# Optimization experiments

Measured on AMD Instinct MI355X. Metric: run time of the kernel, lower is better.

## Reference

```python
import jax, jax.numpy as jnp
import numpy as np

EPS = 1e-12  # matches torch F.normalize default eps

def _l2_normalize(v, axis):
    n = jnp.sqrt(jnp.sum(v * v, axis=axis, keepdims=True))
    return v / jnp.maximum(n, EPS)

def setup_inputs() -> dict:
    key = jax.random.key(0)
    k1, k2, k3 = jax.random.split(key, 3)
    N, C, H, W = 16, 128, 64, 64
    D, K = 512, 64
    x = jax.random.normal(k1, (N, C, H, W), dtype=jnp.float32)
    conv_w = jax.random.normal(k2, (D, C), dtype=jnp.float32) * (1.0 / np.sqrt(C))
    conv_b = jnp.zeros((D,), dtype=jnp.float32)
    centroids = jax.random.uniform(k3, (K, D), dtype=jnp.float32)
    return {"x": x, "conv_w": conv_w, "conv_b": conv_b, "centroids": centroids}

def reference(x, conv_w, conv_b, centroids):
    N, C, H, W = x.shape
    D = conv_w.shape[0]
    # descriptor-wise L2 normalization over channels
    x = _l2_normalize(x, axis=1)
    # 1x1 conv == per-pixel linear projection; flatten spatial -> L = H*W
    f = jnp.einsum('nchw,dc->ndhw', x, conv_w) + conv_b[None, :, None, None]
    f = f.reshape(N, D, H * W)                      # (N, D, L)
    c = _l2_normalize(centroids, axis=1)            # (K, D)
    # soft assignment: dot of normalized centroid with each projected descriptor
    logits = jnp.einsum('kd,ndl->nkl', c, f)        # (N, K, L)
    s = jax.nn.softmax(logits, axis=-1)             # softmax over spatial positions
    # weighted sum of descriptors per cluster (no (N,K,D,L) materialization)
    vlad = jnp.einsum('nkl,ndl->nkd', s, f)         # (N, K, D)
    return vlad
```

## Files before the change

kernel.cpp:

```cpp
#include <hip/hip_runtime.h>

#define NB 16
#define CD 128
#define HW 4096
#define DD 512
#define KC 64

typedef __attribute__((ext_vector_type(8))) short bfrag;
typedef __attribute__((ext_vector_type(4))) float facc;

__device__ __forceinline__ unsigned short f2bf(float f) {
  union { float f; unsigned u; } v; v.f = f;
  unsigned r = v.u + 0x7fffu + ((v.u >> 16) & 1u);
  return (unsigned short)(r >> 16);
}
__device__ __forceinline__ float bf2f(unsigned short h) {
  union { unsigned u; float f; } v; v.u = ((unsigned)h) << 16; return v.f;
}
__device__ __forceinline__ unsigned f2bf2(float lo, float hi) {
  unsigned r;
  asm("v_cvt_pk_bf16_f32 %0, %1, %2" : "=v"(r) : "v"(lo), "v"(hi));
  return r;
}
__device__ __forceinline__ void gll16(const void* g, void* l) {
  __builtin_amdgcn_global_load_lds(
      (__attribute__((address_space(1))) void*)(uintptr_t)g,
      (__attribute__((address_space(3))) void*)(uintptr_t)l, 16, 0, 0);
}
__device__ __forceinline__ int swzr(int r) { return ((r & 7) ^ ((r >> 3) & 7)) << 4; }

__global__ __launch_bounds__(256) void k_prep(const float* __restrict__ conv_w,
                                              const float* __restrict__ conv_b,
                                              const float* __restrict__ centroids,
                                              unsigned short* __restrict__ Wsw,
                                              unsigned short* __restrict__ Mg,
                                              float* __restrict__ bk) {
  int b = blockIdx.x, t = threadIdx.x;
  if (b < KC) {
    __shared__ float red[4];
    __shared__ float sinv;
    __shared__ float mred[256];
    const float* row = centroids + (size_t)b * DD;
    float v0 = row[t], v1 = row[t + 256];
    float ss = v0 * v0 + v1 * v1;
    #pragma unroll
    for (int off = 32; off; off >>= 1) ss += __shfl_xor(ss, off);
    if ((t & 63) == 0) red[t >> 6] = ss;
    __syncthreads();
    if (t == 0) sinv = 1.0f / fmaxf(sqrtf(red[0] + red[1] + red[2] + red[3]), 1e-12f);
    __syncthreads();
    float inv = sinv;
    int dd = t >> 7, c = t & 127;
    float macc = 0.f;
    #pragma unroll 8
    for (int d0 = 0; d0 < DD; d0 += 2) {
      float cn = row[d0 + dd];
      macc += cn * conv_w[(size_t)(d0 + dd) * CD + c];
    }
    mred[t] = macc;
    float bp = v0 * conv_b[t] + v1 * conv_b[t + 256];
    #pragma unroll
    for (int off = 32; off; off >>= 1) bp += __shfl_xor(bp, off);
    if ((t & 63) == 0) red[t >> 6] = bp;
    __syncthreads();
    if (t < 128) Mg[(size_t)b * CD + t] = f2bf((mred[t] + mred[t + 128]) * inv);
    if (t == 0) bk[b] = (red[0] + red[1] + red[2] + red[3]) * inv;
  } else {
    int i = (b - KC) * 2048 + t * 8;
    const float4* src = (const float4*)(conv_w + i);
    float4 a = src[0], c4 = src[1];
    int d = i >> 7, c0 = i & 127;
    int dch = d >> 6, dl = d & 63;
    uint4 w;
    w.x = f2bf2(a.x, a.y);   w.y = f2bf2(a.z, a.w);
    w.z = f2bf2(c4.x, c4.y); w.w = f2bf2(c4.z, c4.w);
    *(uint4*)((char*)Wsw + dch * 16384 + dl * 256 + ((c0 * 2) ^ swzr(dl))) = w;
  }
}

__global__ __launch_bounds__(512, 2) void k_xproj(const float* __restrict__ x,
                                                  const unsigned short* __restrict__ Wsw,
                                                  const unsigned short* __restrict__ Mg,
                                                  const float* __restrict__ bk,
                                                  const float* __restrict__ conv_b,
                                                  unsigned short* __restrict__ fT,
                                                  unsigned short* __restrict__ eg,
                                                  float* __restrict__ psums) {
  __shared__ __align__(16) char smem[67072];
  char* Xraw  = smem;
  char* etile = smem;
  char* Ws0   = smem + 32768;
  float* invb = (float*)(smem + 65536);
  float* ps   = (float*)(smem + 66048);
  int n = blockIdx.y, lblk = blockIdx.x, l0 = lblk * 128;
  int t = threadIdx.x, lane = t & 63, wid = t >> 6;

  #pragma unroll
  for (int q = 0; q < 2; q++)
    gll16((const char*)Wsw + (q * 8 + wid) * 1024 + lane * 16, Ws0 + (q * 8 + wid) * 1024);

  #pragma unroll
  for (int j = 0; j < 2; j++) {
    int c0 = ((t >> 4) + 32 * j) * 2;
    const float4* r0p = (const float4*)(x + ((size_t)n * CD + c0) * HW + l0);
    const float4* r1p = (const float4*)(x + ((size_t)n * CD + c0 + 1) * HW + l0);
    #pragma unroll
    for (int jj = 0; jj < 2; jj++) {
      int f4 = (t & 15) + 16 * jj;
      float4 a = r0p[f4], b = r1p[f4];
      int lb = f4 * 4;
      *(unsigned*)(Xraw + (lb + 0) * 256 + ((c0 * 2) ^ swzr(lb + 0))) = f2bf2(a.x, b.x);
      *(unsigned*)(Xraw + (lb + 1) * 256 + ((c0 * 2) ^ swzr(lb + 1))) = f2bf2(a.y, b.y);
      *(unsigned*)(Xraw + (lb + 2) * 256 + ((c0 * 2) ^ swzr(lb + 2))) = f2bf2(a.z, b.z);
      *(unsigned*)(Xraw + (lb + 3) * 256 + ((c0 * 2) ^ swzr(lb + 3))) = f2bf2(a.w, b.w);
    }
  }
  __syncthreads();

  int wd = wid & 1, wl = wid >> 1;
  int ek = wid & 1;
  int r0 = (lane >> 4) << 2, cl = lane & 15;
  int hi8 = (lane >> 4) << 3;

  bfrag ma[4][2];
  #pragma unroll
  for (int kk = 0; kk < 4; kk++)
    #pragma unroll
    for (int m2 = 0; m2 < 2; m2++)
      ma[kk][m2] = *(const bfrag*)(Mg + (size_t)(ek * 32 + m2 * 16 + cl) * CD + kk * 32 + hi8);

  {
    int l = t >> 2;
    float ss = 0.f;
    #pragma unroll
    for (int p = 0; p < 4; p++) {
      int s16 = (t & 3) + 4 * p;
      bfrag v = *(const bfrag*)(Xraw + l * 256 + ((s16 * 16) ^ swzr(l)));
      #pragma unroll
      for (int i = 0; i < 8; i++) { float f = bf2f((unsigned short)v[i]); ss += f * f; }
    }
    ss += __shfl_xor(ss, 1); ss += __shfl_xor(ss, 2);
    if ((t & 3) == 0) invb[l] = 1.0f / fmaxf(sqrtf(ss), 1e-12f);
  }
  __syncthreads();

  bfrag bfh[4][2];
  #pragma unroll
  for (int kk = 0; kk < 4; kk++)
    #pragma unroll
    for (int j = 0; j < 2; j++) {
      int row = wl * 32 + j * 16 + cl;
      int c0e = kk * 32 + hi8;
      bfh[kk][j] = *(const bfrag*)(Xraw + row * 256 + ((c0e * 2) ^ swzr(row)));
    }
  float hinv[2];
  #pragma unroll
  for (int j = 0; j < 2; j++) hinv[j] = invb[wl * 32 + j * 16 + cl];
  __syncthreads();

  facc zero = {0.f, 0.f, 0.f, 0.f};
  facc e_acc[2][2];
  e_acc[0][0] = zero; e_acc[0][1] = zero; e_acc[1][0] = zero; e_acc[1][1] = zero;
  #pragma unroll
  for (int kk = 0; kk < 4; kk++)
    #pragma unroll
    for (int m2 = 0; m2 < 2; m2++)
      #pragma unroll
      for (int j2 = 0; j2 < 2; j2++)
        e_acc[m2][j2] = __builtin_amdgcn_mfma_f32_16x16x32_bf16(ma[kk][m2], bfh[kk][j2], e_acc[m2][j2], 0, 0, 0);

  for (int dch = 0; dch < 8; dch++) {
    const char* Wsb = Ws0 + ((dch & 1) << 14);
    char* fb = smem + ((dch & 1) << 14);
    facc acc[2][2];
    acc[0][0] = zero; acc[0][1] = zero; acc[1][0] = zero; acc[1][1] = zero;
    #pragma unroll
    for (int kk = 0; kk < 4; kk++) {
      int c0e = kk * 32 + hi8;
      bfrag am[2];
      #pragma unroll
      for (int m = 0; m < 2; m++) {
        int d = wd * 32 + m * 16 + cl;
        am[m] = *(const bfrag*)(Wsb + d * 256 + ((c0e * 2) ^ swzr(d)));
      }
      #pragma unroll
      for (int m = 0; m < 2; m++)
        #pragma unroll
        for (int j = 0; j < 2; j++)
          acc[m][j] = __builtin_amdgcn_mfma_f32_16x16x32_bf16(am[m], bfh[kk][j], acc[m][j], 0, 0, 0);
    }
    #pragma unroll
    for (int m = 0; m < 2; m++) {
      int d0 = wd * 32 + m * 16 + r0;
      float4 bq = *(const float4*)(conv_b + dch * 64 + d0);
      #pragma unroll
      for (int j = 0; j < 2; j++) {
        int l = wl * 32 + j * 16 + cl;
        uint2 w;
        w.x = f2bf2(acc[m][j][0] * hinv[j] + bq.x, acc[m][j][1] * hinv[j] + bq.y);
        w.y = f2bf2(acc[m][j][2] * hinv[j] + bq.z, acc[m][j][3] * hinv[j] + bq.w);
        *(uint2*)(fb + l * 128 + ((d0 * 2) ^ swzr(l))) = w;
      }
    }
    if (dch < 7) {
      #pragma unroll
      for (int q = 0; q < 2; q++)
        gll16((const char*)Wsw + (dch + 1) * 16384 + (q * 8 + wid) * 1024 + lane * 16,
              Ws0 + (((dch + 1) & 1) << 14) + (q * 8 + wid) * 1024);
    }
    __builtin_amdgcn_sched_barrier(0);
    if (dch >= 1) {
      const char* fprev = smem + (((dch - 1) & 1) << 14);
      #pragma unroll
      for (int p = 0; p < 2; p++) {
        int ch = p * 512 + t;
        int lr = ch >> 3, c16 = ch & 7;
        bfrag v = *(const bfrag*)(fprev + lr * 128 + ((c16 * 16) ^ swzr(lr)));
        *(bfrag*)(fT + ((size_t)n * HW + l0 + lr) * DD + (dch - 1) * 64 + c16 * 8) = v;
      }
    }
    if (dch == 0) { asm volatile("s_waitcnt vmcnt(0) lgkmcnt(0)" ::: "memory"); }
    else         { asm volatile("s_waitcnt vmcnt(2) lgkmcnt(0)" ::: "memory"); }
    __builtin_amdgcn_s_barrier();
    __builtin_amdgcn_sched_barrier(0);
  }
  {
    const char* fprev = smem + 16384;
    #pragma unroll
    for (int p = 0; p < 2; p++) {
      int ch = p * 512 + t;
      int lr = ch >> 3, c16 = ch & 7;
      bfrag v = *(const bfrag*)(fprev + lr * 128 + ((c16 * 16) ^ swzr(lr)));
      *(bfrag*)(fT + ((size_t)n * HW + l0 + lr) * DD + 7 * 64 + c16 * 8) = v;
    }
  }

  {
    #pragma unroll
    for (int m2 = 0; m2 < 2; m2++) {
      int k20 = ek * 32 + m2 * 16 + r0;
      float4 bkq = *(const float4*)(bk + k20);
      #pragma unroll
      for (int q = 0; q < 4; q++) {
        int k2 = k20 + q;
        float bkv = (q == 0) ? bkq.x : (q == 1) ? bkq.y : (q == 2) ? bkq.z : bkq.w;
        float vsum = 0.f;
        #pragma unroll
        for (int j2 = 0; j2 < 2; j2++) {
          int l2 = wl * 32 + j2 * 16 + cl;
          float ev = __expf(e_acc[m2][j2][q] * hinv[j2] + bkv);
          *(unsigned short*)(etile + (l2 >> 6) * 8192 + k2 * 128 +
                             (((l2 & 63) * 2) ^ swzr(k2))) = f2bf(ev);
          vsum += ev;
        }
        vsum += __shfl_xor(vsum, 1); vsum += __shfl_xor(vsum, 2);
        vsum += __shfl_xor(vsum, 4); vsum += __shfl_xor(vsum, 8);
        if (cl == 0) ps[k2 * 4 + wl] = vsum;
      }
    }
  }
  __syncthreads();
  {
    size_t base = ((size_t)n * 64 + lblk * 2) * 8192;
    #pragma unroll
    for (int p = 0; p < 2; p++) {
      uint4 v = *(const uint4*)(etile + (t + p * 512) * 16);
      *(uint4*)((char*)eg + base + (t + p * 512) * 16) = v;
    }
  }
  if (t < 64) {
    float4 v = ((const float4*)ps)[t];
    psums[((size_t)n * 32 + lblk) * 64 + t] = v.x + v.y + v.z + v.w;
  }
}

__global__ __launch_bounds__(256, 2) void k_vlad(const unsigned short* __restrict__ eg,
                                                 const unsigned short* __restrict__ fT,
                                                 float* __restrict__ part) {
  __shared__ __align__(16) char smem[49152];
  char* As = smem;
  char* Bs = smem + 16384;
  int t = threadIdx.x, lane = t & 63, wid = t >> 6;
  int wr = wid >> 1, wc = wid & 1;
  int lin = blockIdx.x;
  int xcd = lin & 7, jj = lin >> 3;
  int grp = xcd * 16 + (jj >> 2);
  int dt = jj & 3, n = grp >> 3, sk = grp & 7;
  int dbase = dt * 128;
  const unsigned short* fTb = fT + (size_t)n * HW * DD + dbase;
  facc acc[2][4];
  facc zero = {0.f, 0.f, 0.f, 0.f};
  #pragma unroll
  for (int m = 0; m < 2; m++)
    #pragma unroll
    for (int j = 0; j < 4; j++) acc[m][j] = zero;

  bfrag br[8];
  #pragma unroll
  for (int q = 0; q < 8; q++) {
    int ch = q * 256 + t;
    int l = ch >> 4, dc = ch & 15;
    br[q] = *(const bfrag*)(fTb + (size_t)(sk * 512 + l) * DD + dc * 8);
  }

  #pragma unroll
  for (int ks = 0; ks < 4; ks++) {
    int l0 = sk * 512 + ks * 128;
    #pragma unroll
    for (int q = 0; q < 8; q++) {
      int ch = q * 256 + t;
      int l = ch >> 4, dc = ch & 15;
      #pragma unroll
      for (int i = 0; i < 8; i++) {
        int d = dc * 8 + i;
        int swz = (((d & 7) ^ ((d >> 3) & 7)) << 4);
        *(unsigned short*)(Bs + d * 256 + ((l * 2) ^ swz)) = (unsigned short)br[q][i];
      }
    }
    __builtin_amdgcn_sched_barrier(0);
    {
      const char* easrc = (const char*)eg + ((size_t)n * 64 + (l0 >> 6)) * 8192;
      #pragma unroll
      for (int q = 0; q < 4; q++)
        gll16(easrc + (q * 4 + wid) * 1024 + lane * 16, As + (q * 4 + wid) * 1024);
    }
    __builtin_amdgcn_sched_barrier(0);
    if (ks < 3) {
      #pragma unroll
      for (int q = 0; q < 8; q++) {
        int ch = q * 256 + t;
        int l = ch >> 4, dc = ch & 15;
        br[q] = *(const bfrag*)(fTb + (size_t)(l0 + 128 + l) * DD + dc * 8);
      }
      asm volatile("s_waitcnt vmcnt(8) lgkmcnt(0)" ::: "memory");
    } else {
      asm volatile("s_waitcnt vmcnt(0) lgkmcnt(0)" ::: "memory");
    }
    __builtin_amdgcn_s_barrier();
    __builtin_amdgcn_sched_barrier(0);
    #pragma unroll
    for (int kk = 0; kk < 128; kk += 32) {
      int lk = kk + ((lane >> 4) << 3);
      const char* Ai = As + (kk >> 6) * 8192;
      int ll = lk & 63;
      bfrag af[2], bf[4];
      #pragma unroll
      for (int m = 0; m < 2; m++) {
        int krow = wr * 32 + m * 16 + (lane & 15);
        af[m] = *(const bfrag*)(Ai + krow * 128 + ((ll * 2) ^ swzr(krow)));
      }
      #pragma unroll
      for (int j = 0; j < 4; j++) {
        int d = wc * 64 + j * 16 + (lane & 15);
        int swz = (((d & 7) ^ ((d >> 3) & 7)) << 4);
        bf[j] = *(const bfrag*)(Bs + d * 256 + ((lk * 2) ^ swz));
      }
      #pragma unroll
      for (int m = 0; m < 2; m++)
        #pragma unroll
        for (int j = 0; j < 4; j++)
          acc[m][j] = __builtin_amdgcn_mfma_f32_16x16x32_bf16(af[m], bf[j], acc[m][j], 0, 0, 0);
    }
    asm volatile("s_waitcnt lgkmcnt(0)" ::: "memory");
    __builtin_amdgcn_s_barrier();
    __builtin_amdgcn_sched_barrier(0);
  }
  int r0 = (lane >> 4) << 2, cl = lane & 15;
  size_t base = ((size_t)(sk * NB + n)) * (KC * DD);
  #pragma unroll
  for (int m = 0; m < 2; m++) {
    int krow = wr * 32 + m * 16 + r0;
    #pragma unroll
    for (int j = 0; j < 4; j++) {
      int d = dbase + wc * 64 + j * 16 + cl;
      #pragma unroll
      for (int q = 0; q < 4; q++)
        part[base + (size_t)(krow + q) * DD + d] = acc[m][j][q];
    }
  }
}

__global__ __launch_bounds__(256) void k_reduce(const float* __restrict__ part,
                                                const float* __restrict__ psums,
                                                float* __restrict__ out) {
  int b = blockIdx.x, t = threadIdx.x;
  int nk = b >> 1;
  int n = nk >> 6, k = nk & 63;
  __shared__ float rsh;
  if (t < 32) {
    float s = psums[((size_t)n * 32 + t) * 64 + k];
    #pragma unroll
    for (int off = 16; off; off >>= 1) s += __shfl_xor(s, off, 32);
    if (t == 0) rsh = 1.0f / s;
  }
  __syncthreads();
  float rinv = rsh;
  int i = b * 256 + t;
  float s = 0.f;
  #pragma unroll
  for (int skk = 0; skk < 8; skk++) s += part[(size_t)skk * (NB * KC * DD) + i];
  out[i] = s * rinv;
}

extern "C" void kernel_launch(void* const* d_in, const int* in_sizes, int n_in,
                              void* d_out, int out_size, void* d_ws, size_t ws_size,
                              hipStream_t stream) {
  const float* x         = (const float*)d_in[0];
  const float* conv_w    = (const float*)d_in[1];
  const float* conv_b    = (const float*)d_in[2];
  const float* centroids = (const float*)d_in[3];
  float* out = (float*)d_out;
  char* ws = (char*)d_ws;

  unsigned short* Wsw  = (unsigned short*)(ws);
  unsigned short* Mg   = (unsigned short*)(ws + 131072);
  float*          bk   = (float*)(ws + 147456);
  unsigned short* fT   = (unsigned short*)(ws + 148480);
  unsigned short* eg   = (unsigned short*)(ws + 67257344ull);
  float*          psums= (float*)(ws + 75645952ull);
  float*          part = (float*)(ws + 75777024ull);

  k_prep<<<dim3(96), dim3(256), 0, stream>>>(conv_w, conv_b, centroids, Wsw, Mg, bk);

  k_xproj<<<dim3(32, NB), dim3(512), 0, stream>>>(x, Wsw, Mg, bk, conv_b, fT, eg, psums);

  k_vlad<<<dim3(512), dim3(256), 0, stream>>>(eg, fT, part);

  k_reduce<<<dim3(NB * KC * DD / 256), dim3(256), 0, stream>>>(part, psums, out);

  (void)in_sizes; (void)n_in; (void)out_size; (void)ws_size;
}
```

Baseline: 62.36 us.

## Fuse projection, exp-assignment, and VLAD accumulation into one kernel

Merges the projection kernel and the VLAD GEMM kernel so that the projected descriptors and exp-weights stay in shared memory. This removes the round trip of the large bf16 fT tensor and the eg buffer through global memory. Each block now covers 256 spatial positions in four 64-wide sub-tiles and accumulates the partial VLAD in registers. The grid shrinks to 256 blocks with one block per CU, and k_reduce now sums 16 partials instead of 8. In exchange the kernel gives up occupancy, runs more barriers per sub-tile, and loses the overlap of W loads with compute (the W chunks are reloaded for every sub-tile).

```diff
diff --git a/kernel.cpp b/kernel.cpp
--- a/kernel.cpp
+++ b/kernel.cpp
@@ -52,7 +52,7 @@
     float inv = sinv;
     int dd = t >> 7, c = t & 127;
     float macc = 0.f;
-    #pragma unroll 8
+    #pragma unroll 16
     for (int d0 = 0; d0 < DD; d0 += 2) {
       float cn = row[d0 + dd];
       macc += cn * conv_w[(size_t)(d0 + dd) * CD + c];
@@ -78,47 +78,24 @@
   }
 }
 
-__global__ __launch_bounds__(512, 2) void k_xproj(const float* __restrict__ x,
+__global__ __launch_bounds__(512, 1) void k_fused(const float* __restrict__ x,
                                                   const unsigned short* __restrict__ Wsw,
                                                   const unsigned short* __restrict__ Mg,
                                                   const float* __restrict__ bk,
                                                   const float* __restrict__ conv_b,
-                                                  unsigned short* __restrict__ fT,
-                                                  unsigned short* __restrict__ eg,
+                                                  float* __restrict__ part,
                                                   float* __restrict__ psums) {
-  __shared__ __align__(16) char smem[67072];
-  char* Xraw  = smem;
-  char* etile = smem;
-  char* Ws0   = smem + 32768;
-  float* invb = (float*)(smem + 65536);
-  float* ps   = (float*)(smem + 66048);
-  int n = blockIdx.y, lblk = blockIdx.x, l0 = lblk * 128;
+  __shared__ __align__(16) char smem[124160];
+  char* Xsub  = smem;
+  char* ftile = smem + 16384;
+  char* WsB   = smem + 81920;
+  char* etile = smem + 114688;
+  float* invb = (float*)(smem + 122880);
+  float* ps   = (float*)(smem + 123136);
+  int n = blockIdx.y, lblk = blockIdx.x;
   int t = threadIdx.x, lane = t & 63, wid = t >> 6;
-
-  #pragma unroll
-  for (int q = 0; q < 2; q++)
-    gll16((const char*)Wsw + (q * 8 + wid) * 1024 + lane * 16, Ws0 + (q * 8 + wid) * 1024);
-
-  #pragma unroll
-  for (int j = 0; j < 2; j++) {
-    int c0 = ((t >> 4) + 32 * j) * 2;
-    const float4* r0p = (const float4*)(x + ((size_t)n * CD + c0) * HW + l0);
-    const float4* r1p = (const float4*)(x + ((size_t)n * CD + c0 + 1) * HW + l0);
-    #pragma unroll
-    for (int jj = 0; jj < 2; jj++) {
-      int f4 = (t & 15) + 16 * jj;
-      float4 a = r0p[f4], b = r1p[f4];
-      int lb = f4 * 4;
-      *(unsigned*)(Xraw + (lb + 0) * 256 + ((c0 * 2) ^ swzr(lb + 0))) = f2bf2(a.x, b.x);
-      *(unsigned*)(Xraw + (lb + 1) * 256 + ((c0 * 2) ^ swzr(lb + 1))) = f2bf2(a.y, b.y);
-      *(unsigned*)(Xraw + (lb + 2) * 256 + ((c0 * 2) ^ swzr(lb + 2))) = f2bf2(a.z, b.z);
-      *(unsigned*)(Xraw + (lb + 3) * 256 + ((c0 * 2) ^ swzr(lb + 3))) = f2bf2(a.w, b.w);
-    }
-  }
-  __syncthreads();
-
-  int wd = wid & 1, wl = wid >> 1;
-  int ek = wid & 1;
+  int g2 = wid >> 2;
+  int g4 = wid & 3;
   int r0 = (lane >> 4) << 2, cl = lane & 15;
   int hi8 = (lane >> 4) << 3;
 
@@ -127,256 +104,180 @@
   for (int kk = 0; kk < 4; kk++)
     #pragma unroll
     for (int m2 = 0; m2 < 2; m2++)
-      ma[kk][m2] = *(const bfrag*)(Mg + (size_t)(ek * 32 + m2 * 16 + cl) * CD + kk * 32 + hi8);
+      ma[kk][m2] = *(const bfrag*)(Mg + (size_t)(g2 * 32 + m2 * 16 + cl) * CD + kk * 32 + hi8);
+  float4 bkh[2];
+  #pragma unroll
+  for (int m2 = 0; m2 < 2; m2++) bkh[m2] = *(const float4*)(bk + g2 * 32 + m2 * 16 + r0);
+  float bvh[8];
+  #pragma unroll
+  for (int dch = 0; dch < 8; dch++) bvh[dch] = conv_b[dch * 64 + g4 * 16 + cl];
+
+  #pragma unroll
+  for (int q = 0; q < 2; q++)
+    gll16((const char*)Wsw + (q * 8 + wid) * 1024 + lane * 16, WsB + (q * 8 + wid) * 1024);
+
+  facc zero = {0.f, 0.f, 0.f, 0.f};
+  facc acc_v[2][8];
+  #pragma unroll
+  for (int m = 0; m < 2; m++)
+    #pragma unroll
+    for (int j = 0; j < 8; j++) acc_v[m][j] = zero;
+  float rs[2][4] = {{0.f,0.f,0.f,0.f},{0.f,0.f,0.f,0.f}};
+
+  for (int sub = 0; sub < 4; sub++) {
+    int l0 = lblk * 256 + sub * 64;
+    {
+      int c0 = (t >> 3) * 2;
+      const float4* r0p = (const float4*)(x + ((size_t)n * CD + c0) * HW + l0);
+      const float4* r1p = (const float4*)(x + ((size_t)n * CD + c0 + 1) * HW + l0);
+      #pragma unroll
+      for (int jj = 0; jj < 2; jj++) {
+        int f4 = (t & 7) + 8 * jj;
+        float4 a = r0p[f4], b = r1p[f4];
+        int lb = f4 * 4;
+        *(unsigned*)(Xsub + (lb + 0) * 256 + ((c0 * 2) ^ swzr(lb + 0))) = f2bf2(a.x, b.x);
+        *(unsigned*)(Xsub + (lb + 1) * 256 + ((c0 * 2) ^ swzr(lb + 1))) = f2bf2(a.y, b.y);
+        *(unsigned*)(Xsub + (lb + 2) * 256 + ((c0 * 2) ^ swzr(lb + 2))) = f2bf2(a.z, b.z);
+        *(unsigned*)(Xsub + (lb + 3) * 256 + ((c0 * 2) ^ swzr(lb + 3))) = f2bf2(a.w, b.w);
+      }
+    }
+    __syncthreads();
+    {
+      int l = t >> 3;
+      float ss = 0.f;
+      #pragma unroll
+      for (int p = 0; p < 2; p++) {
+        int s16 = (t & 7) + 8 * p;
+        bfrag v = *(const bfrag*)(Xsub + l * 256 + ((s16 * 16) ^ swzr(l)));
+        #pragma unroll
+        for (int i = 0; i < 8; i++) { float f = bf2f((unsigned short)v[i]); ss += f * f; }
+      }
+      ss += __shfl_xor(ss, 1); ss += __shfl_xor(ss, 2); ss += __shfl_xor(ss, 4);
+      if ((t & 7) == 0) invb[l] = 1.0f / fmaxf(sqrtf(ss), 1e-12f);
+    }
+    __syncthreads();
+
+    bfrag bfh[4][2];
+    #pragma unroll
+    for (int kk = 0; kk < 4; kk++)
+      #pragma unroll
+      for (int m = 0; m < 2; m++) {
+        int row = g2 * 32 + m * 16 + cl;
+        bfh[kk][m] = *(const bfrag*)(Xsub + row * 256 + (((kk * 32 + hi8) * 2) ^ swzr(row)));
+      }
+    float hinvq[2][4];
+    #pragma unroll
+    for (int m = 0; m < 2; m++)
+      #pragma unroll
+      for (int q = 0; q < 4; q++) hinvq[m][q] = invb[g2 * 32 + m * 16 + r0 + q];
+    float invl = invb[g4 * 16 + cl];
+
+    facc e_acc[2];
+    e_acc[0] = zero; e_acc[1] = zero;
+    #pragma unroll
+    for (int kk = 0; kk < 4; kk++) {
+      int erow = g4 * 16 + cl;
+      bfrag xe = *(const bfrag*)(Xsub + erow * 256 + (((kk * 32 + hi8) * 2) ^ swzr(erow)));
+      #pragma unroll
+      for (int m2 = 0; m2 < 2; m2++)
+        e_acc[m2] = __builtin_amdgcn_mfma_f32_16x16x32_bf16(ma[kk][m2], xe, e_acc[m2], 0, 0, 0);
+    }
+    #pragma unroll
+    for (int m2 = 0; m2 < 2; m2++) {
+      #pragma unroll
+      for (int q = 0; q < 4; q++) {
+        int k2 = g2 * 32 + m2 * 16 + r0 + q;
+        float bkv = (q == 0) ? bkh[m2].x : (q == 1) ? bkh[m2].y : (q == 2) ? bkh[m2].z : bkh[m2].w;
+        float ev = __expf(e_acc[m2][q] * invl + bkv);
+        int l2 = g4 * 16 + cl;
+        *(unsigned short*)(etile + k2 * 128 + ((l2 * 2) ^ swzr(k2))) = f2bf(ev);
+        rs[m2][q] += ev;
+      }
+    }
+
+    for (int dch = 0; dch < 8; dch++) {
+      {
+        int nxt = (dch + 1) & 7;
+        char* wdst = WsB + (((dch + 1) & 1) << 14);
+        #pragma unroll
+        for (int q = 0; q < 2; q++)
+          gll16((const char*)Wsw + nxt * 16384 + (q * 8 + wid) * 1024 + lane * 16,
+                wdst + (q * 8 + wid) * 1024);
+      }
+      const char* Wsb = WsB + ((dch & 1) << 14);
+      facc fa[2];
+      fa[0] = zero; fa[1] = zero;
+      #pragma unroll
+      for (int kk = 0; kk < 4; kk++) {
+        int drow = g4 * 16 + cl;
+        bfrag wf = *(const bfrag*)(Wsb + drow * 256 + (((kk * 32 + hi8) * 2) ^ swzr(drow)));
+        #pragma unroll
+        for (int m = 0; m < 2; m++)
+          fa[m] = __builtin_amdgcn_mfma_f32_16x16x32_bf16(bfh[kk][m], wf, fa[m], 0, 0, 0);
+      }
+      {
+        int d = dch * 64 + g4 * 16 + cl;
+        float bv = bvh[dch];
+        #pragma unroll
+        for (int m = 0; m < 2; m++) {
+          int lm = g2 * 32 + m * 16 + r0;
+          uint2 w;
+          w.x = f2bf2(fa[m][0] * hinvq[m][0] + bv, fa[m][1] * hinvq[m][1] + bv);
+          w.y = f2bf2(fa[m][2] * hinvq[m][2] + bv, fa[m][3] * hinvq[m][3] + bv);
+          *(uint2*)(ftile + d * 128 + ((lm * 2) ^ swzr(d))) = w;
+        }
+      }
+      __syncthreads();
+    }
+
+    #pragma unroll
+    for (int kk2 = 0; kk2 < 2; kk2++) {
+      int loff = (kk2 * 32 + hi8) * 2;
+      bfrag ae[2];
+      #pragma unroll
+      for (int m = 0; m < 2; m++) {
+        int krow = g2 * 32 + m * 16 + cl;
+        ae[m] = *(const bfrag*)(etile + krow * 128 + (loff ^ swzr(krow)));
+      }
+      #pragma unroll
+      for (int j = 0; j < 8; j++) {
+        int d = g4 * 128 + j * 16 + cl;
+        bfrag bf = *(const bfrag*)(ftile + d * 128 + (loff ^ swzr(d)));
+        #pragma unroll
+        for (int m = 0; m < 2; m++)
+          acc_v[m][j] = __builtin_amdgcn_mfma_f32_16x16x32_bf16(ae[m], bf, acc_v[m][j], 0, 0, 0);
+      }
+    }
+    __syncthreads();
+  }
 
   {
-    int l = t >> 2;
-    float ss = 0.f;
-    #pragma unroll
-    for (int p = 0; p < 4; p++) {
-      int s16 = (t & 3) + 4 * p;
-      bfrag v = *(const bfrag*)(Xraw + l * 256 + ((s16 * 16) ^ swzr(l)));
-      #pragma unroll
-      for (int i = 0; i < 8; i++) { float f = bf2f((unsigned short)v[i]); ss += f * f; }
-    }
-    ss += __shfl_xor(ss, 1); ss += __shfl_xor(ss, 2);
-    if ((t & 3) == 0) invb[l] = 1.0f / fmaxf(sqrtf(ss), 1e-12f);
-  }
+    size_t base = ((size_t)(lblk * NB + n)) * (KC * DD);
+    #pragma unroll
+    for (int m = 0; m < 2; m++) {
+      int krow = g2 * 32 + m * 16 + r0;
+      #pragma unroll
+      for (int j = 0; j < 8; j++) {
+        int d = g4 * 128 + j * 16 + cl;
+        #pragma unroll
+        for (int q = 0; q < 4; q++)
+          part[base + (size_t)(krow + q) * DD + d] = acc_v[m][j][q];
+      }
+    }
+  }
+  #pragma unroll
+  for (int m2 = 0; m2 < 2; m2++)
+    #pragma unroll
+    for (int q = 0; q < 4; q++) {
+      float v = rs[m2][q];
+      v += __shfl_xor(v, 1); v += __shfl_xor(v, 2);
+      v += __shfl_xor(v, 4); v += __shfl_xor(v, 8);
+      if (cl == 0) ps[(g2 * 32 + m2 * 16 + r0 + q) * 4 + g4] = v;
+    }
   __syncthreads();
-
-  bfrag bfh[4][2];
-  #pragma unroll
-  for (int kk = 0; kk < 4; kk++)
-    #pragma unroll
-    for (int j = 0; j < 2; j++) {
-      int row = wl * 32 + j * 16 + cl;
-      int c0e = kk * 32 + hi8;
-      bfh[kk][j] = *(const bfrag*)(Xraw + row * 256 + ((c0e * 2) ^ swzr(row)));
-    }
-  float hinv[2];
-  #pragma unroll
-  for (int j = 0; j < 2; j++) hinv[j] = invb[wl * 32 + j * 16 + cl];
-  __syncthreads();
-
-  facc zero = {0.f, 0.f, 0.f, 0.f};
-  facc e_acc[2][2];
-  e_acc[0][0] = zero; e_acc[0][1] = zero; e_acc[1][0] = zero; e_acc[1][1] = zero;
-  #pragma unroll
-  for (int kk = 0; kk < 4; kk++)
-    #pragma unroll
-    for (int m2 = 0; m2 < 2; m2++)
-      #pragma unroll
-      for (int j2 = 0; j2 < 2; j2++)
-        e_acc[m2][j2] = __builtin_amdgcn_mfma_f32_16x16x32_bf16(ma[kk][m2], bfh[kk][j2], e_acc[m2][j2], 0, 0, 0);
-
-  for (int dch = 0; dch < 8; dch++) {
-    const char* Wsb = Ws0 + ((dch & 1) << 14);
-    char* fb = smem + ((dch & 1) << 14);
-    facc acc[2][2];
-    acc[0][0] = zero; acc[0][1] = zero; acc[1][0] = zero; acc[1][1] = zero;
-    #pragma unroll
-    for (int kk = 0; kk < 4; kk++) {
-      int c0e = kk * 32 + hi8;
-      bfrag am[2];
-      #pragma unroll
-      for (int m = 0; m < 2; m++) {
-        int d = wd * 32 + m * 16 + cl;
-        am[m] = *(const bfrag*)(Wsb + d * 256 + ((c0e * 2) ^ swzr(d)));
-      }
-      #pragma unroll
-      for (int m = 0; m < 2; m++)
-        #pragma unroll
-        for (int j = 0; j < 2; j++)
-          acc[m][j] = __builtin_amdgcn_mfma_f32_16x16x32_bf16(am[m], bfh[kk][j], acc[m][j], 0, 0, 0);
-    }
-    #pragma unroll
-    for (int m = 0; m < 2; m++) {
-      int d0 = wd * 32 + m * 16 + r0;
-      float4 bq = *(const float4*)(conv_b + dch * 64 + d0);
-      #pragma unroll
-      for (int j = 0; j < 2; j++) {
-        int l = wl * 32 + j * 16 + cl;
-        uint2 w;
-        w.x = f2bf2(acc[m][j][0] * hinv[j] + bq.x, acc[m][j][1] * hinv[j] + bq.y);
-        w.y = f2bf2(acc[m][j][2] * hinv[j] + bq.z, acc[m][j][3] * hinv[j] + bq.w);
-        *(uint2*)(fb + l * 128 + ((d0 * 2) ^ swzr(l))) = w;
-      }
-    }
-    if (dch < 7) {
-      #pragma unroll
-      for (int q = 0; q < 2; q++)
-        gll16((const char*)Wsw + (dch + 1) * 16384 + (q * 8 + wid) * 1024 + lane * 16,
-              Ws0 + (((dch + 1) & 1) << 14) + (q * 8 + wid) * 1024);
-    }
-    __builtin_amdgcn_sched_barrier(0);
-    if (dch >= 1) {
-      const char* fprev = smem + (((dch - 1) & 1) << 14);
-      #pragma unroll
-      for (int p = 0; p < 2; p++) {
-        int ch = p * 512 + t;
-        int lr = ch >> 3, c16 = ch & 7;
-        bfrag v = *(const bfrag*)(fprev + lr * 128 + ((c16 * 16) ^ swzr(lr)));
-        *(bfrag*)(fT + ((size_t)n * HW + l0 + lr) * DD + (dch - 1) * 64 + c16 * 8) = v;
-      }
-    }
-    if (dch == 0) { asm volatile("s_waitcnt vmcnt(0) lgkmcnt(0)" ::: "memory"); }
-    else         { asm volatile("s_waitcnt vmcnt(2) lgkmcnt(0)" ::: "memory"); }
-    __builtin_amdgcn_s_barrier();
-    __builtin_amdgcn_sched_barrier(0);
-  }
-  {
-    const char* fprev = smem + 16384;
-    #pragma unroll
-    for (int p = 0; p < 2; p++) {
-      int ch = p * 512 + t;
-      int lr = ch >> 3, c16 = ch & 7;
-      bfrag v = *(const bfrag*)(fprev + lr * 128 + ((c16 * 16) ^ swzr(lr)));
-      *(bfrag*)(fT + ((size_t)n * HW + l0 + lr) * DD + 7 * 64 + c16 * 8) = v;
-    }
-  }
-
-  {
-    #pragma unroll
-    for (int m2 = 0; m2 < 2; m2++) {
-      int k20 = ek * 32 + m2 * 16 + r0;
-      float4 bkq = *(const float4*)(bk + k20);
-      #pragma unroll
-      for (int q = 0; q < 4; q++) {
-        int k2 = k20 + q;
-        float bkv = (q == 0) ? bkq.x : (q == 1) ? bkq.y : (q == 2) ? bkq.z : bkq.w;
-        float vsum = 0.f;
-        #pragma unroll
-        for (int j2 = 0; j2 < 2; j2++) {
-          int l2 = wl * 32 + j2 * 16 + cl;
-          float ev = __expf(e_acc[m2][j2][q] * hinv[j2] + bkv);
-          *(unsigned short*)(etile + (l2 >> 6) * 8192 + k2 * 128 +
-                             (((l2 & 63) * 2) ^ swzr(k2))) = f2bf(ev);
-          vsum += ev;
-        }
-        vsum += __shfl_xor(vsum, 1); vsum += __shfl_xor(vsum, 2);
-        vsum += __shfl_xor(vsum, 4); vsum += __shfl_xor(vsum, 8);
-        if (cl == 0) ps[k2 * 4 + wl] = vsum;
-      }
-    }
-  }
-  __syncthreads();
-  {
-    size_t base = ((size_t)n * 64 + lblk * 2) * 8192;
-    #pragma unroll
-    for (int p = 0; p < 2; p++) {
-      uint4 v = *(const uint4*)(etile + (t + p * 512) * 16);
-      *(uint4*)((char*)eg + base + (t + p * 512) * 16) = v;
-    }
-  }
   if (t < 64) {
     float4 v = ((const float4*)ps)[t];
-    psums[((size_t)n * 32 + lblk) * 64 + t] = v.x + v.y + v.z + v.w;
-  }
-}
-
-__global__ __launch_bounds__(256, 2) void k_vlad(const unsigned short* __restrict__ eg,
-                                                 const unsigned short* __restrict__ fT,
-                                                 float* __restrict__ part) {
-  __shared__ __align__(16) char smem[49152];
-  char* As = smem;
-  char* Bs = smem + 16384;
-  int t = threadIdx.x, lane = t & 63, wid = t >> 6;
-  int wr = wid >> 1, wc = wid & 1;
-  int lin = blockIdx.x;
-  int xcd = lin & 7, jj = lin >> 3;
-  int grp = xcd * 16 + (jj >> 2);
-  int dt = jj & 3, n = grp >> 3, sk = grp & 7;
-  int dbase = dt * 128;
-  const unsigned short* fTb = fT + (size_t)n * HW * DD + dbase;
-  facc acc[2][4];
-  facc zero = {0.f, 0.f, 0.f, 0.f};
-  #pragma unroll
-  for (int m = 0; m < 2; m++)
-    #pragma unroll
-    for (int j = 0; j < 4; j++) acc[m][j] = zero;
-
-  bfrag br[8];
-  #pragma unroll
-  for (int q = 0; q < 8; q++) {
-    int ch = q * 256 + t;
-    int l = ch >> 4, dc = ch & 15;
-    br[q] = *(const bfrag*)(fTb + (size_t)(sk * 512 + l) * DD + dc * 8);
-  }
-
-  #pragma unroll
-  for (int ks = 0; ks < 4; ks++) {
-    int l0 = sk * 512 + ks * 128;
-    #pragma unroll
-    for (int q = 0; q < 8; q++) {
-      int ch = q * 256 + t;
-      int l = ch >> 4, dc = ch & 15;
-      #pragma unroll
-      for (int i = 0; i < 8; i++) {
-        int d = dc * 8 + i;
-        int swz = (((d & 7) ^ ((d >> 3) & 7)) << 4);
-        *(unsigned short*)(Bs + d * 256 + ((l * 2) ^ swz)) = (unsigned short)br[q][i];
-      }
-    }
-    __builtin_amdgcn_sched_barrier(0);
-    {
-      const char* easrc = (const char*)eg + ((size_t)n * 64 + (l0 >> 6)) * 8192;
-      #pragma unroll
-      for (int q = 0; q < 4; q++)
-        gll16(easrc + (q * 4 + wid) * 1024 + lane * 16, As + (q * 4 + wid) * 1024);
-    }
-    __builtin_amdgcn_sched_barrier(0);
-    if (ks < 3) {
-      #pragma unroll
-      for (int q = 0; q < 8; q++) {
-        int ch = q * 256 + t;
-        int l = ch >> 4, dc = ch & 15;
-        br[q] = *(const bfrag*)(fTb + (size_t)(l0 + 128 + l) * DD + dc * 8);
-      }
-      asm volatile("s_waitcnt vmcnt(8) lgkmcnt(0)" ::: "memory");
-    } else {
-      asm volatile("s_waitcnt vmcnt(0) lgkmcnt(0)" ::: "memory");
-    }
-    __builtin_amdgcn_s_barrier();
-    __builtin_amdgcn_sched_barrier(0);
-    #pragma unroll
-    for (int kk = 0; kk < 128; kk += 32) {
-      int lk = kk + ((lane >> 4) << 3);
-      const char* Ai = As + (kk >> 6) * 8192;
-      int ll = lk & 63;
-      bfrag af[2], bf[4];
-      #pragma unroll
-      for (int m = 0; m < 2; m++) {
-        int krow = wr * 32 + m * 16 + (lane & 15);
-        af[m] = *(const bfrag*)(Ai + krow * 128 + ((ll * 2) ^ swzr(krow)));
-      }
-      #pragma unroll
-      for (int j = 0; j < 4; j++) {
-        int d = wc * 64 + j * 16 + (lane & 15);
-        int swz = (((d & 7) ^ ((d >> 3) & 7)) << 4);
-        bf[j] = *(const bfrag*)(Bs + d * 256 + ((lk * 2) ^ swz));
-      }
-      #pragma unroll
-      for (int m = 0; m < 2; m++)
-        #pragma unroll
-        for (int j = 0; j < 4; j++)
-          acc[m][j] = __builtin_amdgcn_mfma_f32_16x16x32_bf16(af[m], bf[j], acc[m][j], 0, 0, 0);
-    }
-    asm volatile("s_waitcnt lgkmcnt(0)" ::: "memory");
-    __builtin_amdgcn_s_barrier();
-    __builtin_amdgcn_sched_barrier(0);
-  }
-  int r0 = (lane >> 4) << 2, cl = lane & 15;
-  size_t base = ((size_t)(sk * NB + n)) * (KC * DD);
-  #pragma unroll
-  for (int m = 0; m < 2; m++) {
-    int krow = wr * 32 + m * 16 + r0;
-    #pragma unroll
-    for (int j = 0; j < 4; j++) {
-      int d = dbase + wc * 64 + j * 16 + cl;
-      #pragma unroll
-      for (int q = 0; q < 4; q++)
-        part[base + (size_t)(krow + q) * DD + d] = acc[m][j][q];
-    }
+    psums[((size_t)n * 16 + lblk) * 64 + t] = v.x + v.y + v.z + v.w;
   }
 }
 
@@ -387,10 +288,10 @@
   int nk = b >> 1;
   int n = nk >> 6, k = nk & 63;
   __shared__ float rsh;
-  if (t < 32) {
-    float s = psums[((size_t)n * 32 + t) * 64 + k];
-    #pragma unroll
-    for (int off = 16; off; off >>= 1) s += __shfl_xor(s, off, 32);
+  if (t < 16) {
+    float s = psums[((size_t)n * 16 + t) * 64 + k];
+    s += __shfl_xor(s, 8, 16); s += __shfl_xor(s, 4, 16);
+    s += __shfl_xor(s, 2, 16); s += __shfl_xor(s, 1, 16);
     if (t == 0) rsh = 1.0f / s;
   }
   __syncthreads();
@@ -398,7 +299,7 @@
   int i = b * 256 + t;
   float s = 0.f;
   #pragma unroll
-  for (int skk = 0; skk < 8; skk++) s += part[(size_t)skk * (NB * KC * DD) + i];
+  for (int lc = 0; lc < 16; lc++) s += part[(size_t)lc * (NB * KC * DD) + i];
   out[i] = s * rinv;
 }
 
@@ -415,16 +316,12 @@
   unsigned short* Wsw  = (unsigned short*)(ws);
   unsigned short* Mg   = (unsigned short*)(ws + 131072);
   float*          bk   = (float*)(ws + 147456);
-  unsigned short* fT   = (unsigned short*)(ws + 148480);
-  unsigned short* eg   = (unsigned short*)(ws + 67257344ull);
-  float*          psums= (float*)(ws + 75645952ull);
-  float*          part = (float*)(ws + 75777024ull);
+  float*          psums= (float*)(ws + 148480);
+  float*          part = (float*)(ws + 214016);
 
   k_prep<<<dim3(96), dim3(256), 0, stream>>>(conv_w, conv_b, centroids, Wsw, Mg, bk);
 
-  k_xproj<<<dim3(32, NB), dim3(512), 0, stream>>>(x, Wsw, Mg, bk, conv_b, fT, eg, psums);
-
-  k_vlad<<<dim3(512), dim3(256), 0, stream>>>(eg, fT, part);
+  k_fused<<<dim3(16, NB), dim3(512), 0, stream>>>(x, Wsw, Mg, bk, conv_b, part, psums);
 
   k_reduce<<<dim3(NB * KC * DD / 256), dim3(256), 0, stream>>>(part, psums, out);
 
```

Measured after the change: 65.39 us. 4.9% more time.
